# Kernel optimization log

Measured on AMD Instinct MI355X. Metric: run time of the kernel, lower is better.

The kernel has to match this reference:

```python
import jax, jax.numpy as jnp
import numpy as np

NEG_BIG = -2.0**32 + 1.0  # padding value used by the torch module


def setup_inputs() -> dict:
    key = jax.random.key(0)
    k1, k2, k3, k4 = jax.random.split(key, 4)
    B, T, D = 8, 1024, 1024
    x = jax.random.normal(k1, (B, T, D), dtype=jnp.float32)
    mask = jnp.ones((B, T), dtype=jnp.float32)
    Wq = jax.random.normal(k2, (D, D), dtype=jnp.float32) * 0.02
    Wk = jax.random.normal(k3, (D, D), dtype=jnp.float32) * 0.02
    Wv = jax.random.normal(k4, (D, D), dtype=jnp.float32) * 0.02
    return {"x": x, "mask": mask, "Wq": Wq, "Wk": Wk, "Wv": Wv}


def reference(x, mask, Wq, Wk, Wv):
    # direction = FORWARD, dropout = 0.0, n_heads = 8
    n_heads = 8
    B, T, D = x.shape
    d = D // n_heads

    # nn.Linear(bias=False): y = x @ W.T
    Q = x @ Wq.T
    K = x @ Wk.T
    V = x @ Wv.T

    # torch.cat(torch.split(Q, d, dim=2), dim=0) -> [h*B, T, d], head-major
    def heads(t):
        return t.reshape(B, T, n_heads, d).transpose(2, 0, 1, 3)  # (h,B,T,d)

    Qh, Kh, Vh = heads(Q), heads(K), heads(V)

    scores = jnp.einsum('hbqd,hbkd->hbqk', Qh, Kh) / jnp.sqrt(jnp.float32(d))

    # key padding mask from K_ itself
    key_masks = jnp.sign(jnp.sum(jnp.abs(Kh), axis=-1))  # (h,B,T)
    scores = jnp.where(key_masks[:, :, None, :] == 0, jnp.float32(NEG_BIG), scores)

    # FORWARD direction: sw_col[i,j]=i, sw_row[i,j]=j; mask = (j > i) -> strict upper tri
    dir_mask = jnp.triu(jnp.ones((T, T), dtype=jnp.float32), k=1)
    adder = (1.0 - dir_mask) * -10000.0
    scores = scores + adder  # broadcasts over (h,B)

    attn = jax.nn.softmax(scores, axis=-1)

    query_masks = jnp.sign(jnp.sum(jnp.abs(Qh), axis=-1))  # (h,B,T)
    attn = attn * query_masks[:, :, :, None]

    out = jnp.einsum('hbqk,hbkd->hbqd', attn, Vh)  # (h,B,T,d)
    out = out.transpose(1, 2, 0, 3).reshape(B, T, D)  # cat heads back on feature dim

    out = out * mask[:, :, None]
    return out
```

## Files before the change

kernel.cpp:

```cpp
#include <hip/hip_runtime.h>
#include <hip/hip_bf16.h>
#include <stdint.h>


typedef __attribute__((ext_vector_type(8))) short short8;
typedef __attribute__((ext_vector_type(4))) float floatx4;

__device__ __forceinline__ short f2bf(float f) {
    union { float f; uint32_t u; } v; v.f = f;
    uint32_t r = v.u + 0x7fffu + ((v.u >> 16) & 1u);
    return (short)(r >> 16);
}
__device__ __forceinline__ float bf2f(short u) {
    union { float f; uint32_t x; } v; v.x = ((uint32_t)(uint16_t)u) << 16;
    return v.f;
}

__device__ __forceinline__ void load_lds_16B(const void* g, void* l) {
    __builtin_amdgcn_global_load_lds(
        (const __attribute__((address_space(1))) void*)g,
        (__attribute__((address_space(3))) void*)l, 16, 0, 0);
}

__global__ __launch_bounds__(256) void cast_all_kernel(
    const float* __restrict__ x, const float* __restrict__ w0,
    const float* __restrict__ w1, const float* __restrict__ w2,
    short* __restrict__ xb, short* __restrict__ wb)
{
    int bid = blockIdx.x;
    const float* src;
    short* dst;
    int i;
    if (bid < 4096) {
        src = x; dst = xb; i = bid * 256 + threadIdx.x;
    } else {
        int sel = (bid - 4096) >> 9;
        int blk = (bid - 4096) & 511;
        src = (sel == 0) ? w0 : ((sel == 1) ? w1 : w2);
        dst = wb + sel * 1048576;
        i = blk * 256 + threadIdx.x;
    }
    float4 a = *(const float4*)(src + i * 8);
    float4 b = *(const float4*)(src + i * 8 + 4);
    short8 o;
    o[0] = f2bf(a.x); o[1] = f2bf(a.y); o[2] = f2bf(a.z); o[3] = f2bf(a.w);
    o[4] = f2bf(b.x); o[5] = f2bf(b.y); o[6] = f2bf(b.z); o[7] = f2bf(b.w);
    *(short8*)(dst + i * 8) = o;
}

__global__ __launch_bounds__(256) void qkv_gemm_kernel(
    const short* __restrict__ xb, const short* __restrict__ wb,
    short* __restrict__ Qh, short* __restrict__ Kh, short* __restrict__ VhT)
{
    __shared__ short smem[16384];
    short* As = smem;
    short* Bs = smem + 8192;
    short* Cs = smem;

    const int tid = threadIdx.x;
    const int m0 = blockIdx.x * 128;
    const int n0 = blockIdx.y * 128;
    const int wave = tid >> 6;
    const int lane = tid & 63;
    const int wm = (wave >> 1) * 64;
    const int wn = (wave & 1) * 64;
    const int l16 = lane & 15;
    const int quad = lane >> 4;
    const int srow = lane >> 2;
    const int scb = ((lane & 3) ^ ((lane >> 3) & 3)) * 8;
    const int rq  = (quad ^ ((l16 >> 1) & 3)) * 8;

    floatx4 zero = {0.0f, 0.0f, 0.0f, 0.0f};
    floatx4 acc[4][4];
    for (int i = 0; i < 4; ++i)
        for (int j = 0; j < 4; ++j) acc[i][j] = zero;

    auto stage = [&](int k0, int bf) {
        #pragma unroll
        for (int c = 0; c < 4; ++c) {
            int chunk = wave * 4 + c;
            if (chunk < 8)
                load_lds_16B(xb + (m0 + chunk * 16 + srow) * 1024 + k0 + scb,
                             &As[bf * 4096 + chunk * 512]);
            else
                load_lds_16B(wb + (n0 + (chunk - 8) * 16 + srow) * 1024 + k0 + scb,
                             &Bs[bf * 4096 + (chunk - 8) * 512]);
        }
    };

    stage(0, 0);
    int buf = 0;
    for (int k0 = 0; k0 < 1024; k0 += 32) {
        __syncthreads();
        if (k0 + 32 < 1024) stage(k0 + 32, buf ^ 1);

        short8 a[4], b[4];
        #pragma unroll
        for (int i = 0; i < 4; ++i)
            a[i] = *(const short8*)&As[buf * 4096 + (wm + i * 16 + l16) * 32 + rq];
        #pragma unroll
        for (int j = 0; j < 4; ++j)
            b[j] = *(const short8*)&Bs[buf * 4096 + (wn + j * 16 + l16) * 32 + rq];
        #pragma unroll
        for (int i = 0; i < 4; ++i)
            #pragma unroll
            for (int j = 0; j < 4; ++j)
                acc[i][j] = __builtin_amdgcn_mfma_f32_16x16x32_bf16(a[i], b[j], acc[i][j], 0, 0, 0);
        buf ^= 1;
    }

    const float qscale = 0.08838834764831845f;
    const int f0 = n0 & 1023;
    const int h = f0 >> 7;
    const bool isV = (n0 >= 2048);
    const float sc = (n0 < 1024) ? qscale : 1.0f;
    short* dst = (n0 < 1024) ? Qh : Kh;

    #pragma unroll
    for (int half = 0; half < 2; ++half) {
        __syncthreads();
        if ((wave >> 1) == half) {
            #pragma unroll
            for (int i = 0; i < 4; ++i)
                #pragma unroll
                for (int j = 0; j < 4; ++j)
                    #pragma unroll
                    for (int p = 0; p < 4; ++p) {
                        int mr = i * 16 + quad * 4 + p;
                        int c = wn + j * 16 + l16;
                        short v = f2bf(acc[i][j][p] * sc);
                        if (isV) Cs[c * 68 + mr] = v;
                        else     Cs[mr * 132 + c] = v;
                    }
        }
        __syncthreads();
        if (!isV) {
            #pragma unroll
            for (int jj = 0; jj < 4; ++jj) {
                int idx = tid + jj * 256;
                int row = idx >> 4;
                int chunk = idx & 15;
                int m = m0 + half * 64 + row;
                int bb = m >> 10, t = m & 1023;
                *(short8*)&dst[((h * 8 + bb) * 1024 + t) * 128 + chunk * 8] =
                    *(const short8*)&Cs[row * 132 + chunk * 8];
            }
        } else {
            int m = m0 + half * 64;
            int bb = m >> 10, t = m & 1023;
            #pragma unroll
            for (int jj = 0; jj < 4; ++jj) {
                int idx = tid + jj * 256;
                int dd = idx >> 3;
                int chunk = idx & 7;
                *(short8*)&VhT[((h * 8 + bb) * 128 + dd) * 1024 + t + chunk * 8] =
                    *(const short8*)&Cs[dd * 68 + chunk * 8];
            }
        }
    }
}

#define LDP 70

__global__ __launch_bounds__(256) void attn_kernel(
    const short* __restrict__ Qh, const short* __restrict__ Kh,
    const short* __restrict__ VhT, const float* __restrict__ mask,
    float* __restrict__ out)
{
    __shared__ short Kb[2][8192];
    __shared__ short Vb[2][8192];
    __shared__ short Ps[4 * 16 * LDP];

    const int tid = threadIdx.x;
    const int hb = blockIdx.x;
    const int qt = blockIdx.y;
    const int h = hb >> 3, b = hb & 7;
    const int base = hb * 131072;

    if (qt == 8) {
        float* qv = (float*)&Kb[0][0];
        float* ps = qv + 128;
        float* red = ps + 1024;
        const int wave = tid >> 6, lane = tid & 63;

        if (tid < 128) qv[tid] = bf2f(Qh[base + 1023 * 128 + tid]);
        __syncthreads();

        float tot = 0.0f;
        #pragma unroll
        for (int kk = 0; kk < 4; ++kk) {
            int k = tid * 4 + kk;
            const short8* kr = (const short8*)(Kh + base + k * 128);
            float acc = 0.0f;
            #pragma unroll
            for (int c = 0; c < 16; ++c) {
                short8 v = kr[c];
                #pragma unroll
                for (int j = 0; j < 8; ++j) acc += qv[c * 8 + j] * bf2f(v[j]);
            }
            float e = __expf(acc);
            ps[k] = e;
            tot += e;
        }
        #pragma unroll
        for (int off = 32; off >= 1; off >>= 1) tot += __shfl_xor(tot, off);
        if (lane == 0) red[wave] = tot;
        __syncthreads();
        float inv = 1.0f / (red[0] + red[1] + red[2] + red[3]);
        inv *= mask[b * 1024 + 1023];

        int dd = tid >> 1, half = tid & 1;
        const short* vr = VhT + base + dd * 1024 + half * 512;
        const float* pp = ps + half * 512;
        float acc = 0.0f;
        for (int k = 0; k < 512; k += 8) {
            short8 v = *(const short8*)(vr + k);
            #pragma unroll
            for (int j = 0; j < 8; ++j) acc += pp[k + j] * bf2f(v[j]);
        }
        acc += __shfl_xor(acc, 1);
        if (half == 0)
            out[(b * 1024 + 1023) * 1024 + h * 128 + dd] = acc * inv;
        return;
    }

    const int wave = tid >> 6;
    const int lane = tid & 63;
    const int l16 = lane & 15;
    const int quad = lane >> 4;
    const int srow = lane >> 2;
    const int scb = ((lane & 3) ^ ((lane >> 3) & 3)) * 8;
    const int rq  = (quad ^ ((l16 >> 1) & 3)) * 8;

    const short* Qp = Qh + base;
    const short* Kp = Kh + base;
    const short* VTp = VhT + base;
    short* Pw = &Ps[wave * 16 * LDP];

    const int q0_lo = qt * 64 + wave * 16;
    const int q0_hi = (15 - qt) * 64 + wave * 16;
    const int hi_start = 15 - qt;

    short8 aq_lo[4], aq_hi[4];
    #pragma unroll
    for (int kk = 0; kk < 4; ++kk) {
        aq_lo[kk] = *(const short8*)(Qp + (q0_lo + l16) * 128 + kk * 32 + quad * 8);
        aq_hi[kk] = *(const short8*)(Qp + (q0_hi + l16) * 128 + kk * 32 + quad * 8);
    }

    floatx4 zero = {0.0f, 0.0f, 0.0f, 0.0f};
    floatx4 o_lo[8], o_hi[8];
    #pragma unroll
    for (int n = 0; n < 8; ++n) { o_lo[n] = zero; o_hi[n] = zero; }
    float l_lo[4] = {0, 0, 0, 0}, l_hi[4] = {0, 0, 0, 0};

    auto stage = [&](int kt, int bf) {
        #pragma unroll
        for (int c = 0; c < 4; ++c) {
            int L = wave * 4 + c;
            int kk = L >> 2, rg = L & 3;
            load_lds_16B(Kp + (kt * 64 + rg * 16 + srow) * 128 + kk * 32 + scb,
                         &Kb[bf][kk * 2048 + rg * 512]);
        }
        #pragma unroll
        for (int c = 0; c < 4; ++c) {
            int L = wave * 4 + c;
            int kk2 = L >> 3, g = L & 7;
            load_lds_16B(VTp + (g * 16 + srow) * 1024 + kt * 64 + kk2 * 32 + scb,
                         &Vb[bf][kk2 * 4096 + g * 512]);
        }
    };

    auto s_phase = [&](int bf, const short8* aq, floatx4* s) {
        #pragma unroll
        for (int sub = 0; sub < 4; ++sub) {
            s[sub] = zero;
            #pragma unroll
            for (int kk = 0; kk < 4; ++kk) {
                short8 bk = *(const short8*)&Kb[bf][kk * 2048 + (sub * 16 + l16) * 32 + rq];
                s[sub] = __builtin_amdgcn_mfma_f32_16x16x32_bf16(aq[kk], bk, s[sub], 0, 0, 0);
            }
        }
    };
    auto exp_phase = [&](floatx4* s, int q0g, float* l, int kt) {
        #pragma unroll
        for (int sub = 0; sub < 4; ++sub)
            #pragma unroll
            for (int p = 0; p < 4; ++p) {
                int qg = q0g + quad * 4 + p;
                int kg = kt * 64 + sub * 16 + l16;
                float sv = s[sub][p];
                if (kg <= qg && qg != 1023) sv -= 10000.0f;
                float e = __expf(sv);
                l[p] += e;
                Pw[(quad * 4 + p) * LDP + sub * 16 + l16] = f2bf(e);
            }
    };
    auto pv_phase = [&](int bf, floatx4* o) {
        #pragma unroll
        for (int kk2 = 0; kk2 < 2; ++kk2) {
            short8 ap = *(const short8*)&Pw[l16 * LDP + kk2 * 32 + quad * 8];
            #pragma unroll
            for (int n = 0; n < 8; ++n) {
                short8 bv = *(const short8*)&Vb[bf][kk2 * 4096 + (n * 16 + l16) * 32 + rq];
                o[n] = __builtin_amdgcn_mfma_f32_16x16x32_bf16(ap, bv, o[n], 0, 0, 0);
            }
        }
    };

    stage(qt, 0);
    int buf = 0;
    for (int kt = qt; kt < 16; ++kt) {
        __syncthreads();
        if (kt + 1 < 16) stage(kt + 1, buf ^ 1);
        const bool do_hi = (kt >= hi_start);
        floatx4 s_lo[4], s_hi[4];
        s_phase(buf, aq_lo, s_lo);
        exp_phase(s_lo, q0_lo, l_lo, kt);
        if (do_hi) s_phase(buf, aq_hi, s_hi);
        pv_phase(buf, o_lo);
        if (do_hi) {
            exp_phase(s_hi, q0_hi, l_hi, kt);
            pv_phase(buf, o_hi);
        }
        buf ^= 1;
    }

    #pragma unroll
    for (int off = 8; off >= 1; off >>= 1)
        #pragma unroll
        for (int p = 0; p < 4; ++p) {
            l_lo[p] += __shfl_xor(l_lo[p], off);
            l_hi[p] += __shfl_xor(l_hi[p], off);
        }

    #pragma unroll
    for (int p = 0; p < 4; ++p) {
        int qg = q0_lo + quad * 4 + p;
        float s = (1.0f / l_lo[p]) * mask[b * 1024 + qg];
        #pragma unroll
        for (int n = 0; n < 8; ++n)
            out[(b * 1024 + qg) * 1024 + h * 128 + n * 16 + l16] = o_lo[n][p] * s;
    }
    #pragma unroll
    for (int p = 0; p < 4; ++p) {
        int qg = q0_hi + quad * 4 + p;
        if (qg == 1023) continue;
        float s = (1.0f / l_hi[p]) * mask[b * 1024 + qg];
        #pragma unroll
        for (int n = 0; n < 8; ++n)
            out[(b * 1024 + qg) * 1024 + h * 128 + n * 16 + l16] = o_hi[n][p] * s;
    }
}

extern "C" void kernel_launch(void* const* d_in, const int* in_sizes, int n_in,
                              void* d_out, int out_size, void* d_ws, size_t ws_size,
                              hipStream_t stream) {
    const float* x    = (const float*)d_in[0];
    const float* mask = (const float*)d_in[1];
    const float* Wq   = (const float*)d_in[2];
    const float* Wk   = (const float*)d_in[3];
    const float* Wv   = (const float*)d_in[4];
    float* out = (float*)d_out;

    short* xb  = (short*)d_ws;
    short* wb  = xb + 8388608;
    short* Qh  = wb + 3145728;
    short* Kh  = Qh + 8388608;
    short* VhT = Kh + 8388608;

    cast_all_kernel<<<5632, 256, 0, stream>>>(x, Wq, Wk, Wv, xb, wb);
    qkv_gemm_kernel<<<dim3(64, 24), 256, 0, stream>>>(xb, wb, Qh, Kh, VhT);
    attn_kernel<<<dim3(64, 9), 256, 0, stream>>>(Qh, Kh, VhT, mask, out);
}
```

Before: 238.2 us.

## Share K/V fragment loads across lo/hi query tiles and use exp2 softmax

```diff
diff --git a/kernel.cpp b/kernel.cpp
--- a/kernel.cpp
+++ b/kernel.cpp
@@ -21,6 +21,9 @@
         (const __attribute__((address_space(1))) void*)g,
         (__attribute__((address_space(3))) void*)l, 16, 0, 0);
 }
+
+#define LOG2E 1.4426950408889634f
+#define NEG_BIAS (-14426.950408889634f)
 
 __global__ __launch_bounds__(256) void cast_all_kernel(
     const float* __restrict__ x, const float* __restrict__ w0,
@@ -109,7 +112,7 @@
         buf ^= 1;
     }
 
-    const float qscale = 0.08838834764831845f;
+    const float qscale = 0.08838834764831845f * LOG2E;
     const int f0 = n0 & 1023;
     const int h = f0 >> 7;
     const bool isV = (n0 >= 2048);
@@ -168,8 +171,9 @@
     float* __restrict__ out)
 {
     __shared__ short Kb[2][8192];
-    __shared__ short Vb[2][8192];
-    __shared__ short Ps[4 * 16 * LDP];
+    __shared__ short Vb[8192];
+    __shared__ short PsL[4 * 16 * LDP];
+    __shared__ short PsH[4 * 16 * LDP];
 
     const int tid = threadIdx.x;
     const int hb = blockIdx.x;
@@ -198,7 +202,7 @@
                 #pragma unroll
                 for (int j = 0; j < 8; ++j) acc += qv[c * 8 + j] * bf2f(v[j]);
             }
-            float e = __expf(acc);
+            float e = __builtin_amdgcn_exp2f(acc);
             ps[k] = e;
             tot += e;
         }
@@ -235,7 +239,8 @@
     const short* Qp = Qh + base;
     const short* Kp = Kh + base;
     const short* VTp = VhT + base;
-    short* Pw = &Ps[wave * 16 * LDP];
+    short* PwL = &PsL[wave * 16 * LDP];
+    short* PwH = &PsH[wave * 16 * LDP];
 
     const int q0_lo = qt * 64 + wave * 16;
     const int q0_hi = (15 - qt) * 64 + wave * 16;
@@ -254,7 +259,7 @@
     for (int n = 0; n < 8; ++n) { o_lo[n] = zero; o_hi[n] = zero; }
     float l_lo[4] = {0, 0, 0, 0}, l_hi[4] = {0, 0, 0, 0};
 
-    auto stage = [&](int kt, int bf) {
+    auto stage_K = [&](int kt, int bf) {
         #pragma unroll
         for (int c = 0; c < 4; ++c) {
             int L = wave * 4 + c;
@@ -262,27 +267,18 @@
             load_lds_16B(Kp + (kt * 64 + rg * 16 + srow) * 128 + kk * 32 + scb,
                          &Kb[bf][kk * 2048 + rg * 512]);
         }
+    };
+    auto stage_V = [&](int kt) {
         #pragma unroll
         for (int c = 0; c < 4; ++c) {
             int L = wave * 4 + c;
             int kk2 = L >> 3, g = L & 7;
             load_lds_16B(VTp + (g * 16 + srow) * 1024 + kt * 64 + kk2 * 32 + scb,
-                         &Vb[bf][kk2 * 4096 + g * 512]);
+                         &Vb[kk2 * 4096 + g * 512]);
         }
     };
 
-    auto s_phase = [&](int bf, const short8* aq, floatx4* s) {
-        #pragma unroll
-        for (int sub = 0; sub < 4; ++sub) {
-            s[sub] = zero;
-            #pragma unroll
-            for (int kk = 0; kk < 4; ++kk) {
-                short8 bk = *(const short8*)&Kb[bf][kk * 2048 + (sub * 16 + l16) * 32 + rq];
-                s[sub] = __builtin_amdgcn_mfma_f32_16x16x32_bf16(aq[kk], bk, s[sub], 0, 0, 0);
-            }
-        }
-    };
-    auto exp_phase = [&](floatx4* s, int q0g, float* l, int kt) {
+    auto exp_phase = [&](floatx4* s, int q0g, float* l, int kt, short* Pw) {
         #pragma unroll
         for (int sub = 0; sub < 4; ++sub)
             #pragma unroll
@@ -290,38 +286,71 @@
                 int qg = q0g + quad * 4 + p;
                 int kg = kt * 64 + sub * 16 + l16;
                 float sv = s[sub][p];
-                if (kg <= qg && qg != 1023) sv -= 10000.0f;
-                float e = __expf(sv);
+                if (kg <= qg && qg != 1023) sv += NEG_BIAS;
+                float e = __builtin_amdgcn_exp2f(sv);
                 l[p] += e;
                 Pw[(quad * 4 + p) * LDP + sub * 16 + l16] = f2bf(e);
             }
     };
-    auto pv_phase = [&](int bf, floatx4* o) {
-        #pragma unroll
-        for (int kk2 = 0; kk2 < 2; ++kk2) {
-            short8 ap = *(const short8*)&Pw[l16 * LDP + kk2 * 32 + quad * 8];
-            #pragma unroll
-            for (int n = 0; n < 8; ++n) {
-                short8 bv = *(const short8*)&Vb[bf][kk2 * 4096 + (n * 16 + l16) * 32 + rq];
-                o[n] = __builtin_amdgcn_mfma_f32_16x16x32_bf16(ap, bv, o[n], 0, 0, 0);
-            }
-        }
-    };
-
-    stage(qt, 0);
+
+    stage_K(qt, 0);
     int buf = 0;
     for (int kt = qt; kt < 16; ++kt) {
         __syncthreads();
-        if (kt + 1 < 16) stage(kt + 1, buf ^ 1);
+        stage_V(kt);
+        if (kt + 1 < 16) stage_K(kt + 1, buf ^ 1);
+
         const bool do_hi = (kt >= hi_start);
         floatx4 s_lo[4], s_hi[4];
-        s_phase(buf, aq_lo, s_lo);
-        exp_phase(s_lo, q0_lo, l_lo, kt);
-        if (do_hi) s_phase(buf, aq_hi, s_hi);
-        pv_phase(buf, o_lo);
         if (do_hi) {
-            exp_phase(s_hi, q0_hi, l_hi, kt);
-            pv_phase(buf, o_hi);
+            #pragma unroll
+            for (int sub = 0; sub < 4; ++sub) {
+                s_lo[sub] = zero; s_hi[sub] = zero;
+                #pragma unroll
+                for (int kk = 0; kk < 4; ++kk) {
+                    short8 bk = *(const short8*)&Kb[buf][kk * 2048 + (sub * 16 + l16) * 32 + rq];
+                    s_lo[sub] = __builtin_amdgcn_mfma_f32_16x16x32_bf16(aq_lo[kk], bk, s_lo[sub], 0, 0, 0);
+                    s_hi[sub] = __builtin_amdgcn_mfma_f32_16x16x32_bf16(aq_hi[kk], bk, s_hi[sub], 0, 0, 0);
+                }
+            }
+            exp_phase(s_lo, q0_lo, l_lo, kt, PwL);
+            exp_phase(s_hi, q0_hi, l_hi, kt, PwH);
+        } else {
+            #pragma unroll
+            for (int sub = 0; sub < 4; ++sub) {
+                s_lo[sub] = zero;
+                #pragma unroll
+                for (int kk = 0; kk < 4; ++kk) {
+                    short8 bk = *(const short8*)&Kb[buf][kk * 2048 + (sub * 16 + l16) * 32 + rq];
+                    s_lo[sub] = __builtin_amdgcn_mfma_f32_16x16x32_bf16(aq_lo[kk], bk, s_lo[sub], 0, 0, 0);
+                }
+            }
+            exp_phase(s_lo, q0_lo, l_lo, kt, PwL);
+        }
+
+        __syncthreads();
+        if (do_hi) {
+            #pragma unroll
+            for (int kk2 = 0; kk2 < 2; ++kk2) {
+                short8 apL = *(const short8*)&PwL[l16 * LDP + kk2 * 32 + quad * 8];
+                short8 apH = *(const short8*)&PwH[l16 * LDP + kk2 * 32 + quad * 8];
+                #pragma unroll
+                for (int n = 0; n < 8; ++n) {
+                    short8 bv = *(const short8*)&Vb[kk2 * 4096 + (n * 16 + l16) * 32 + rq];
+                    o_lo[n] = __builtin_amdgcn_mfma_f32_16x16x32_bf16(apL, bv, o_lo[n], 0, 0, 0);
+                    o_hi[n] = __builtin_amdgcn_mfma_f32_16x16x32_bf16(apH, bv, o_hi[n], 0, 0, 0);
+                }
+            }
+        } else {
+            #pragma unroll
+            for (int kk2 = 0; kk2 < 2; ++kk2) {
+                short8 apL = *(const short8*)&PwL[l16 * LDP + kk2 * 32 + quad * 8];
+                #pragma unroll
+                for (int n = 0; n < 8; ++n) {
+                    short8 bv = *(const short8*)&Vb[kk2 * 4096 + (n * 16 + l16) * 32 + rq];
+                    o_lo[n] = __builtin_amdgcn_mfma_f32_16x16x32_bf16(apL, bv, o_lo[n], 0, 0, 0);
+                }
+            }
         }
         buf ^= 1;
     }
```

New measurement: 246.1 us. +3.3%, slower.
